# Performance work log

Hardware: AMD Instinct MI355X
Metric: run time of the kernel (lower is better)

The kernel has to match this reference:

```python
import jax, jax.numpy as jnp
import numpy as np

NUM_HEADS = 16
HEAD_DIM = 64
INPUT_DIM = 1024
EMBED_DIM = NUM_HEADS * HEAD_DIM  # 1024


def setup_inputs() -> dict:
    key = jax.random.key(0)
    ks = jax.random.split(key, 9)
    B, S = 4, 2048
    scale = 1.0 / np.sqrt(INPUT_DIM)
    return {
        "q": jax.random.normal(ks[0], (B, S, INPUT_DIM), dtype=jnp.float32),
        "k": jax.random.normal(ks[1], (B, S, INPUT_DIM), dtype=jnp.float32),
        "v": jax.random.normal(ks[2], (B, S, INPUT_DIM), dtype=jnp.float32),
        "Wq": jax.random.normal(ks[3], (INPUT_DIM, EMBED_DIM), dtype=jnp.float32) * scale,
        "bq": jax.random.normal(ks[4], (EMBED_DIM,), dtype=jnp.float32) * 0.02,
        "Wk": jax.random.normal(ks[5], (INPUT_DIM, EMBED_DIM), dtype=jnp.float32) * scale,
        "bk": jax.random.normal(ks[6], (EMBED_DIM,), dtype=jnp.float32) * 0.02,
        "Wv": jax.random.normal(ks[7], (INPUT_DIM, EMBED_DIM), dtype=jnp.float32) * scale,
        "bv": jax.random.normal(ks[8], (EMBED_DIM,), dtype=jnp.float32) * 0.02,
    }


def reference(q, k, v, Wq, bq, Wk, bk, Wv, bv):
    B, Sq, _ = q.shape
    Sk = k.shape[1]
    # QKV projections (dropout_prob=0 -> identity; ReLU on value path)
    query = (q @ Wq + bq).reshape(B, Sq, NUM_HEADS, HEAD_DIM).transpose(0, 2, 1, 3)  # [B,H,Sq,D]
    key_ = (k @ Wk + bk).reshape(B, Sk, NUM_HEADS, HEAD_DIM).transpose(0, 2, 1, 3)   # [B,H,Sk,D]
    value = jax.nn.relu(v @ Wv + bv).reshape(B, Sk, NUM_HEADS, HEAD_DIM).transpose(0, 2, 1, 3)
    scores = jnp.einsum("bhqd,bhkd->bhqk", query, key_) / np.sqrt(HEAD_DIM).astype(np.float32)
    p_attn = jax.nn.softmax(scores, axis=-1)
    x = jnp.einsum("bhqk,bhkd->bhqd", p_attn, value)  # [B,H,Sq,D]
    return x.transpose(0, 2, 1, 3).reshape(B, Sq, EMBED_DIM)
```

## Files before the change

### kernel.cpp

```cpp
#include <hip/hip_runtime.h>
#include <hip/hip_bf16.h>
#include <stdint.h>

#define BB    4
#define NH    16
#define SEQ   2048
#define DH    64
#define EMB   1024
#define KD    1024
#define MROWS 8192

typedef short  short8  __attribute__((ext_vector_type(8)));
typedef float  f32x4   __attribute__((ext_vector_type(4)));
typedef float  f32x16  __attribute__((ext_vector_type(16)));

typedef const __attribute__((address_space(1))) void* gas_t;
typedef __attribute__((address_space(3))) void*       las_t;
#define GLD16(g, l) __builtin_amdgcn_global_load_lds((gas_t)(g), (las_t)(l), 16, 0, 0)

__device__ __forceinline__ unsigned short f2bf(float f) {
    unsigned u = __float_as_uint(f);
    u += 0x7fffu + ((u >> 16) & 1u);
    return (unsigned short)(u >> 16);
}
__device__ __forceinline__ unsigned packbf(float lo, float hi) {
    union { __hip_bfloat162 h; unsigned u; } cv;
    cv.h = __float22bfloat162_rn(make_float2(lo, hi));
    return cv.u;
}

__global__ __launch_bounds__(256) void wt_kernel(const float* __restrict__ Wq,
                                                 const float* __restrict__ Wk,
                                                 const float* __restrict__ Wv,
                                                 unsigned short* __restrict__ Wt) {
    __shared__ float tsh[64 * 68];
    const int p = blockIdx.z;
    const float* W = (p == 0) ? Wq : (p == 1) ? Wk : Wv;
    unsigned short* dst = Wt + (size_t)p * (KD * EMB);
    const int k0 = blockIdx.x * 64, n0 = blockIdx.y * 64;
    const int t = threadIdx.x;
    {
        const int r = t >> 2, c4 = (t & 3) * 16;
        const float* g = W + (size_t)(k0 + r) * EMB + n0 + c4;
        float* row = &tsh[r * 68 + c4];
        *(float4*)(row + 0)  = *(const float4*)(g + 0);
        *(float4*)(row + 4)  = *(const float4*)(g + 4);
        *(float4*)(row + 8)  = *(const float4*)(g + 8);
        *(float4*)(row + 12) = *(const float4*)(g + 12);
    }
    __syncthreads();
    {
        const int j = t >> 2, kp = (t & 3) * 16;
        unsigned ub[8];
#pragma unroll
        for (int ii = 0; ii < 8; ++ii)
            ub[ii] = packbf(tsh[(kp + 2 * ii) * 68 + j], tsh[(kp + 2 * ii + 1) * 68 + j]);
        unsigned short* o = dst + (size_t)(n0 + j) * KD + k0 + kp;
        *(uint4*)(o + 0) = uint4{ub[0], ub[1], ub[2], ub[3]};
        *(uint4*)(o + 8) = uint4{ub[4], ub[5], ub[6], ub[7]};
    }
}

__global__ __launch_bounds__(256) void proj_kernel(
    const float* __restrict__ qf, const float* __restrict__ kf,
    const float* __restrict__ vf, const unsigned short* __restrict__ WtBase,
    const float* __restrict__ bq, const float* __restrict__ bk, const float* __restrict__ bv,
    unsigned short* __restrict__ Qg, unsigned short* __restrict__ Kg,
    unsigned short* __restrict__ Vt)
{
    __shared__ __align__(16) unsigned short smem[17408];
    unsigned short* Ash = smem;
    unsigned short* Bsh = smem + 8192;

    const int p = blockIdx.z;
    const float* Af = (p == 0) ? qf : (p == 1) ? kf : vf;
    const unsigned short* Wp  = WtBase  + (size_t)p * (KD * EMB);
    const float* bias = (p == 0) ? bq : (p == 1) ? bk : bv;
    unsigned short* dst = (p == 0) ? Qg : (p == 1) ? Kg : Vt;

    const int row0 = blockIdx.x * 128;
    const int col0 = blockIdx.y * 128;
    const int t = threadIdx.x, lane = t & 63, wv = t >> 6;
    const int ln15 = lane & 15, q4 = lane >> 4;
    const int wm = wv & 1, wn = wv >> 1;

    f32x4 acc[4][4];
#pragma unroll
    for (int i = 0; i < 4; ++i)
#pragma unroll
        for (int j = 0; j < 4; ++j)
#pragma unroll
            for (int r = 0; r < 4; ++r) acc[i][j][r] = 0.f;

    const int lr = lane >> 3, lc = (lane & 7) ^ lr;
    const float*          gAf = Af + (size_t)(row0 + wv * 32 + lr) * KD + lc * 8;
    const unsigned short* gB  = Wp + (size_t)(col0 + wv * 32 + lr) * KD + lc * 8;
    unsigned short* lA = Ash + wv * 32 * 64;
    unsigned short* lB = Bsh + wv * 32 * 64;

    for (int k0 = 0; k0 < KD; k0 += 64) {
#pragma unroll
        for (int i = 0; i < 4; ++i) {
            GLD16(gB + (size_t)i * 8 * KD + k0, lB + i * 512);
            float4 a0 = *(const float4*)(gAf + (size_t)i * 8 * KD + k0);
            float4 a1 = *(const float4*)(gAf + (size_t)i * 8 * KD + k0 + 4);
            uint4 u;
            u.x = packbf(a0.x, a0.y); u.y = packbf(a0.z, a0.w);
            u.z = packbf(a1.x, a1.y); u.w = packbf(a1.z, a1.w);
            *(uint4*)&lA[i * 512 + lane * 8] = u;
        }
        __syncthreads();
#pragma unroll
        for (int kk = 0; kk < 2; ++kk) {
            short8 af[4], bfr[4];
#pragma unroll
            for (int mi = 0; mi < 4; ++mi) {
                const int r = wm * 64 + mi * 16 + ln15;
                af[mi] = *(const short8*)&Ash[r * 64 + (((kk << 2) | q4) ^ (r & 7)) * 8];
            }
#pragma unroll
            for (int ni = 0; ni < 4; ++ni) {
                const int r = wn * 64 + ni * 16 + ln15;
                bfr[ni] = *(const short8*)&Bsh[r * 64 + (((kk << 2) | q4) ^ (r & 7)) * 8];
            }
#pragma unroll
            for (int mi = 0; mi < 4; ++mi)
#pragma unroll
                for (int ni = 0; ni < 4; ++ni)
                    acc[mi][ni] = __builtin_amdgcn_mfma_f32_16x16x32_bf16(
                        af[mi], bfr[ni], acc[mi][ni], 0, 0, 0);
        }
        __syncthreads();
    }

    float bvv[4];
#pragma unroll
    for (int ni = 0; ni < 4; ++ni) bvv[ni] = bias[col0 + wn * 64 + ni * 16 + ln15];
    const float scq = 0.18033688011112042f;

    unsigned short* Tsh = smem;
#pragma unroll
    for (int mi = 0; mi < 4; ++mi)
#pragma unroll
        for (int ni = 0; ni < 4; ++ni)
#pragma unroll
            for (int r = 0; r < 4; ++r) {
                const int mr = wm * 64 + mi * 16 + q4 * 4 + r;
                const int ec = wn * 64 + ni * 16 + ln15;
                float vv = acc[mi][ni][r] + bvv[ni];
                if (p == 0) vv *= scq;
                if (p == 2) vv = vv > 0.f ? vv : 0.f;
                Tsh[mr * 136 + ec] = f2bf(vv);
            }
    __syncthreads();

    if (p < 2) {
        const int mr = t >> 1, hsel = t & 1;
        const int m = row0 + mr, bi = m >> 11, s = m & 2047;
        const int hh = (col0 >> 6) + hsel;
        const unsigned short* src = &Tsh[mr * 136 + hsel * 64];
        unsigned short* o = dst + ((size_t)(bi * NH + hh) * SEQ + s) * DH;
#pragma unroll
        for (int c = 0; c < 8; ++c)
            *(uint4*)(o + 8 * c) = *(const uint4*)(src + 8 * c);
    } else {
        const int e = t >> 1, sh2 = t & 1;
        const int n = col0 + e, hh = n >> 6, dd = n & 63;
        const int bi = row0 >> 11, sbase = (row0 & 2047) + sh2 * 64;
        unsigned ub[32];
#pragma unroll
        for (int i = 0; i < 32; ++i)
            ub[i] = (unsigned)Tsh[(sh2 * 64 + 2 * i) * 136 + e] |
                    ((unsigned)Tsh[(sh2 * 64 + 2 * i + 1) * 136 + e] << 16);
        unsigned short* o = dst + ((size_t)(bi * NH + hh) * DH + dd) * SEQ + sbase;
#pragma unroll
        for (int c = 0; c < 8; ++c)
            *(uint4*)(o + 8 * c) = uint4{ub[4 * c], ub[4 * c + 1], ub[4 * c + 2], ub[4 * c + 3]};
    }
}

__global__ __launch_bounds__(512) void attn_kernel(
    const unsigned short* __restrict__ Qg, const unsigned short* __restrict__ Kg,
    const unsigned short* __restrict__ Vt, float* __restrict__ out)
{
    __shared__ __align__(16) unsigned short smem[18432];

    const int lin = blockIdx.x + (blockIdx.y << 3) + (blockIdx.z << 7);
    const int g_xcd = lin & 7, s_lin = lin >> 3;
    const int qb = s_lin & 7;
    const int bh_idx = g_xcd + ((s_lin >> 3) << 3);
    const int hh = bh_idx & 15, bb = bh_idx >> 4;

    const int t = threadIdx.x, lane = t & 63, wv = t >> 6;
    const int ln31 = lane & 31, h2 = lane >> 5;
    const size_t bh = (size_t)(bb * NH + hh);
    const unsigned short* Qp = Qg + bh * (SEQ * DH);
    const unsigned short* Kp = Kg + bh * (SEQ * DH);
    const unsigned short* Vp = Vt + bh * (DH * SEQ);
    const int q0 = qb * 256 + wv * 32;

    short8 qf[4];
#pragma unroll
    for (int dc = 0; dc < 4; ++dc)
        qf[dc] = *(const short8*)(Qp + (size_t)(q0 + ln31) * DH + h2 * 8 + dc * 16);

    short8 ones;
#pragma unroll
    for (int i = 0; i < 8; ++i) ones[i] = (short)0x3F80;

    f32x16 accO[2], accL;
#pragma unroll
    for (int i = 0; i < 16; ++i) { accO[0][i] = 0.f; accO[1][i] = 0.f; accL[i] = 0.f; }

    const int srow = t >> 3, sp = (t & 7) * 8;
    const int prow = srow ^ (((((srow >> 2) ^ (srow >> 3)) & 1)) ? 12 : 0);
    const unsigned short* gk = Kp + (size_t)srow * DH + sp;
    const unsigned short* gv = Vp + (size_t)srow * SEQ + sp;
    const int wkoff = prow * 72 + sp;
    const int wvoff = 4608 + srow * 72 + sp;

    {
        short8 ka = *(const short8*)(gk);
        short8 va = *(const short8*)(gv);
        *(short8*)&smem[wkoff] = ka;
        *(short8*)&smem[wvoff] = va;
    }

    for (int it = 0; it < 32; ++it) {
        const int nxt = (it + 1) & 31;
        short8 ka = *(const short8*)(gk + (size_t)nxt * 64 * DH);
        short8 va = *(const short8*)(gv + nxt * 64);

        __syncthreads();

        const unsigned short* Ksh = smem + (it & 1) * 9216;
        const unsigned short* Vsh = Ksh + 4608;

        f32x16 st[2];
#pragma unroll
        for (int kt = 0; kt < 2; ++kt) {
#pragma unroll
            for (int i = 0; i < 16; ++i) st[kt][i] = 0.f;
#pragma unroll
            for (int dc = 0; dc < 4; ++dc) {
                short8 kf = *(const short8*)&Ksh[(kt * 32 + ln31) * 72 + h2 * 8 + dc * 16];
                st[kt] = __builtin_amdgcn_mfma_f32_32x32x16_bf16(kf, qf[dc], st[kt], 0, 0, 0);
            }
        }
#pragma unroll
        for (int kt = 0; kt < 2; ++kt)
#pragma unroll
            for (int r = 0; r < 16; ++r)
                st[kt][r] = __builtin_amdgcn_exp2f(st[kt][r]);

#pragma unroll
        for (int kt = 0; kt < 2; ++kt)
#pragma unroll
            for (int kc = 0; kc < 2; ++kc) {
                union { unsigned u[4]; short8 v; } pf;
#pragma unroll
                for (int i = 0; i < 4; ++i)
                    pf.u[i] = packbf(st[kt][8 * kc + 2 * i], st[kt][8 * kc + 2 * i + 1]);
                accL = __builtin_amdgcn_mfma_f32_32x32x16_bf16(ones, pf.v, accL, 0, 0, 0);
#pragma unroll
                for (int dt = 0; dt < 2; ++dt) {
                    short8 vf = *(const short8*)&Vsh[(dt * 32 + ln31) * 72 + kt * 32 + kc * 16 + h2 * 8];
                    accO[dt] = __builtin_amdgcn_mfma_f32_32x32x16_bf16(vf, pf.v, accO[dt], 0, 0, 0);
                }
            }

        unsigned short* wbuf = smem + ((it + 1) & 1) * 9216;
        *(short8*)&wbuf[wkoff] = ka;
        *(short8*)&wbuf[wvoff] = va;
    }

    const float inv = 1.0f / accL[0];
    float* orow = out + ((size_t)(bb * SEQ + q0 + ln31) * NH + hh) * 64;
#pragma unroll
    for (int dt = 0; dt < 2; ++dt)
#pragma unroll
        for (int g = 0; g < 4; ++g) {
            float4 w;
            w.x = accO[dt][4 * g + 0] * inv;
            w.y = accO[dt][4 * g + 1] * inv;
            w.z = accO[dt][4 * g + 2] * inv;
            w.w = accO[dt][4 * g + 3] * inv;
            *(float4*)(orow + dt * 32 + 4 * h2 + 8 * g) = w;
        }
}

extern "C" void kernel_launch(void* const* d_in, const int* in_sizes, int n_in,
                              void* d_out, int out_size, void* d_ws, size_t ws_size,
                              hipStream_t stream) {
    const float* qf = (const float*)d_in[0];
    const float* kf = (const float*)d_in[1];
    const float* vf = (const float*)d_in[2];
    const float* Wq = (const float*)d_in[3];
    const float* bq = (const float*)d_in[4];
    const float* Wk = (const float*)d_in[5];
    const float* bk = (const float*)d_in[6];
    const float* Wv = (const float*)d_in[7];
    const float* bv = (const float*)d_in[8];

    char* ws = (char*)d_ws;
    unsigned short* Wt  = (unsigned short*)ws;
    unsigned short* Qg  = (unsigned short*)(ws + 6291456);
    unsigned short* Kg  = Qg + 8388608;
    unsigned short* Vt  = Kg + 8388608;
    float* out = (float*)d_out;

    wt_kernel<<<dim3(16, 16, 3), 256, 0, stream>>>(Wq, Wk, Wv, Wt);
    proj_kernel<<<dim3(64, 8, 3), 256, 0, stream>>>(qf, kf, vf, Wt, bq, bk, bv, Qg, Kg, Vt);
    attn_kernel<<<dim3(8, 16, 4), 512, 0, stream>>>(Qg, Kg, Vt, out);
}
```

Measured before the change: 306.1 us.

## Double-buffer LDS and prefetch fp32 A tiles two steps ahead in projection GEMM

Reworks the projection GEMM main loop to ping-pong between two LDS buffers. Weight tiles for the next k-step are loaded asynchronously, and fp32 activations are prefetched into registers two steps ahead and converted to bf16 one step ahead. This overlaps global loads with MFMA work and drops one barrier per iteration. In exchange it doubles shared memory to 64 KB per block and raises register pressure from the prefetch arrays, which may lower occupancy.

```diff
diff --git a/kernel.cpp b/kernel.cpp
--- a/kernel.cpp
+++ b/kernel.cpp
@@ -68,9 +68,7 @@
     unsigned short* __restrict__ Qg, unsigned short* __restrict__ Kg,
     unsigned short* __restrict__ Vt)
 {
-    __shared__ __align__(16) unsigned short smem[17408];
-    unsigned short* Ash = smem;
-    unsigned short* Bsh = smem + 8192;
+    __shared__ __align__(16) unsigned short smem[32768];
 
     const int p = blockIdx.z;
     const float* Af = (p == 0) ? qf : (p == 1) ? kf : vf;
@@ -95,33 +93,55 @@
     const int lr = lane >> 3, lc = (lane & 7) ^ lr;
     const float*          gAf = Af + (size_t)(row0 + wv * 32 + lr) * KD + lc * 8;
     const unsigned short* gB  = Wp + (size_t)(col0 + wv * 32 + lr) * KD + lc * 8;
-    unsigned short* lA = Ash + wv * 32 * 64;
-    unsigned short* lB = Bsh + wv * 32 * 64;
-
-    for (int k0 = 0; k0 < KD; k0 += 64) {
+    const int lAoff = wv * 2048 + lane * 8;
+    const int lBoff = 8192 + wv * 2048;
+
+    float4 aN[4][2];
+    float4 aF[4][2];
+
+    {
+        float4 a0[4][2];
 #pragma unroll
         for (int i = 0; i < 4; ++i) {
-            GLD16(gB + (size_t)i * 8 * KD + k0, lB + i * 512);
-            float4 a0 = *(const float4*)(gAf + (size_t)i * 8 * KD + k0);
-            float4 a1 = *(const float4*)(gAf + (size_t)i * 8 * KD + k0 + 4);
+            a0[i][0] = *(const float4*)(gAf + (size_t)i * 8 * KD + 0);
+            a0[i][1] = *(const float4*)(gAf + (size_t)i * 8 * KD + 4);
+        }
+#pragma unroll
+        for (int i = 0; i < 4; ++i)
+            GLD16(gB + (size_t)i * 8 * KD + 0, smem + lBoff + i * 512);
+#pragma unroll
+        for (int i = 0; i < 4; ++i) {
             uint4 u;
-            u.x = packbf(a0.x, a0.y); u.y = packbf(a0.z, a0.w);
-            u.z = packbf(a1.x, a1.y); u.w = packbf(a1.z, a1.w);
-            *(uint4*)&lA[i * 512 + lane * 8] = u;
-        }
+            u.x = packbf(a0[i][0].x, a0[i][0].y); u.y = packbf(a0[i][0].z, a0[i][0].w);
+            u.z = packbf(a0[i][1].x, a0[i][1].y); u.w = packbf(a0[i][1].z, a0[i][1].w);
+            *(uint4*)&smem[lAoff + i * 512] = u;
+        }
+#pragma unroll
+        for (int i = 0; i < 4; ++i) {
+            aN[i][0] = *(const float4*)(gAf + (size_t)i * 8 * KD + 64);
+            aN[i][1] = *(const float4*)(gAf + (size_t)i * 8 * KD + 64 + 4);
+        }
+    }
+
+#pragma unroll
+    for (int k0 = 0; k0 < 16; ++k0) {
         __syncthreads();
+
+        const unsigned short* Ab_ = smem + (k0 & 1) * 16384;
+        const unsigned short* Bb_ = Ab_ + 8192;
+
 #pragma unroll
         for (int kk = 0; kk < 2; ++kk) {
             short8 af[4], bfr[4];
 #pragma unroll
             for (int mi = 0; mi < 4; ++mi) {
                 const int r = wm * 64 + mi * 16 + ln15;
-                af[mi] = *(const short8*)&Ash[r * 64 + (((kk << 2) | q4) ^ (r & 7)) * 8];
+                af[mi] = *(const short8*)&Ab_[r * 64 + (((kk << 2) | q4) ^ (r & 7)) * 8];
             }
 #pragma unroll
             for (int ni = 0; ni < 4; ++ni) {
                 const int r = wn * 64 + ni * 16 + ln15;
-                bfr[ni] = *(const short8*)&Bsh[r * 64 + (((kk << 2) | q4) ^ (r & 7)) * 8];
+                bfr[ni] = *(const short8*)&Bb_[r * 64 + (((kk << 2) | q4) ^ (r & 7)) * 8];
             }
 #pragma unroll
             for (int mi = 0; mi < 4; ++mi)
@@ -130,8 +150,31 @@
                     acc[mi][ni] = __builtin_amdgcn_mfma_f32_16x16x32_bf16(
                         af[mi], bfr[ni], acc[mi][ni], 0, 0, 0);
         }
-        __syncthreads();
-    }
+
+        if (k0 < 15) {
+            unsigned short* dBuf = smem + ((k0 + 1) & 1) * 16384;
+#pragma unroll
+            for (int i = 0; i < 4; ++i)
+                GLD16(gB + (size_t)i * 8 * KD + (k0 + 1) * 64, dBuf + lBoff + i * 512);
+            if (k0 < 14) {
+#pragma unroll
+                for (int i = 0; i < 4; ++i) {
+                    aF[i][0] = *(const float4*)(gAf + (size_t)i * 8 * KD + (k0 + 2) * 64);
+                    aF[i][1] = *(const float4*)(gAf + (size_t)i * 8 * KD + (k0 + 2) * 64 + 4);
+                }
+            }
+#pragma unroll
+            for (int i = 0; i < 4; ++i) {
+                uint4 u;
+                u.x = packbf(aN[i][0].x, aN[i][0].y); u.y = packbf(aN[i][0].z, aN[i][0].w);
+                u.z = packbf(aN[i][1].x, aN[i][1].y); u.w = packbf(aN[i][1].z, aN[i][1].w);
+                *(uint4*)&dBuf[lAoff + i * 512] = u;
+            }
+#pragma unroll
+            for (int i = 0; i < 4; ++i) { aN[i][0] = aF[i][0]; aN[i][1] = aF[i][1]; }
+        }
+    }
+    __syncthreads();
 
     float bvv[4];
 #pragma unroll
```

New measurement: 321.7 us. +5.1%, slower.

## Widen projection GEMM tile to 128x256 with 512 threads

Applied to the files above, without the earlier changes.

The projection kernel now computes a 128x256 output tile per block with 8 waves instead of 128x128 with 4 waves. The fp32 activation tile, converted to bf16, is shared across twice as many output columns, which halves redundant reads and conversions of the A operand. The epilogue writes the tile back in two 128-column halves through shared memory. In exchange the grid has half as many blocks and uses more LDS per block, which may lower occupancy and add extra syncs in the epilogue.

```diff
diff --git a/kernel.cpp b/kernel.cpp
--- a/kernel.cpp
+++ b/kernel.cpp
@@ -61,14 +61,14 @@
     }
 }
 
-__global__ __launch_bounds__(256) void proj_kernel(
+__global__ __launch_bounds__(512) void proj_kernel(
     const float* __restrict__ qf, const float* __restrict__ kf,
     const float* __restrict__ vf, const unsigned short* __restrict__ WtBase,
     const float* __restrict__ bq, const float* __restrict__ bk, const float* __restrict__ bv,
     unsigned short* __restrict__ Qg, unsigned short* __restrict__ Kg,
     unsigned short* __restrict__ Vt)
 {
-    __shared__ __align__(16) unsigned short smem[17408];
+    __shared__ __align__(16) unsigned short smem[24576];
     unsigned short* Ash = smem;
     unsigned short* Bsh = smem + 8192;
 
@@ -79,10 +79,11 @@
     unsigned short* dst = (p == 0) ? Qg : (p == 1) ? Kg : Vt;
 
     const int row0 = blockIdx.x * 128;
-    const int col0 = blockIdx.y * 128;
+    const int col0 = blockIdx.y * 256;
     const int t = threadIdx.x, lane = t & 63, wv = t >> 6;
     const int ln15 = lane & 15, q4 = lane >> 4;
     const int wm = wv & 1, wn = wv >> 1;
+    const int wva = wv >> 1;
 
     f32x4 acc[4][4];
 #pragma unroll
@@ -93,23 +94,26 @@
             for (int r = 0; r < 4; ++r) acc[i][j][r] = 0.f;
 
     const int lr = lane >> 3, lc = (lane & 7) ^ lr;
-    const float*          gAf = Af + (size_t)(row0 + wv * 32 + lr) * KD + lc * 8;
+    const float*          gAf = Af + (size_t)(row0 + wva * 32 + lr) * KD + lc * 8;
     const unsigned short* gB  = Wp + (size_t)(col0 + wv * 32 + lr) * KD + lc * 8;
-    unsigned short* lA = Ash + wv * 32 * 64;
     unsigned short* lB = Bsh + wv * 32 * 64;
 
     for (int k0 = 0; k0 < KD; k0 += 64) {
 #pragma unroll
-        for (int i = 0; i < 4; ++i) {
+        for (int i = 0; i < 4; ++i)
             GLD16(gB + (size_t)i * 8 * KD + k0, lB + i * 512);
-            float4 a0 = *(const float4*)(gAf + (size_t)i * 8 * KD + k0);
-            float4 a1 = *(const float4*)(gAf + (size_t)i * 8 * KD + k0 + 4);
+#pragma unroll
+        for (int j = 0; j < 2; ++j) {
+            const int i2 = (wv & 1) * 2 + j;
+            float4 a0 = *(const float4*)(gAf + (size_t)i2 * 8 * KD + k0);
+            float4 a1 = *(const float4*)(gAf + (size_t)i2 * 8 * KD + k0 + 4);
             uint4 u;
             u.x = packbf(a0.x, a0.y); u.y = packbf(a0.z, a0.w);
             u.z = packbf(a1.x, a1.y); u.w = packbf(a1.z, a1.w);
-            *(uint4*)&lA[i * 512 + lane * 8] = u;
-        }
-        __syncthreads();
+            *(uint4*)&Ash[wva * 2048 + i2 * 512 + lane * 8] = u;
+        }
+        __syncthreads();
+
 #pragma unroll
         for (int kk = 0; kk < 2; ++kk) {
             short8 af[4], bfr[4];
@@ -140,42 +144,50 @@
 
     unsigned short* Tsh = smem;
 #pragma unroll
-    for (int mi = 0; mi < 4; ++mi)
-#pragma unroll
-        for (int ni = 0; ni < 4; ++ni)
-#pragma unroll
-            for (int r = 0; r < 4; ++r) {
-                const int mr = wm * 64 + mi * 16 + q4 * 4 + r;
-                const int ec = wn * 64 + ni * 16 + ln15;
-                float vv = acc[mi][ni][r] + bvv[ni];
-                if (p == 0) vv *= scq;
-                if (p == 2) vv = vv > 0.f ? vv : 0.f;
-                Tsh[mr * 136 + ec] = f2bf(vv);
-            }
-    __syncthreads();
-
-    if (p < 2) {
-        const int mr = t >> 1, hsel = t & 1;
-        const int m = row0 + mr, bi = m >> 11, s = m & 2047;
-        const int hh = (col0 >> 6) + hsel;
-        const unsigned short* src = &Tsh[mr * 136 + hsel * 64];
-        unsigned short* o = dst + ((size_t)(bi * NH + hh) * SEQ + s) * DH;
-#pragma unroll
-        for (int c = 0; c < 8; ++c)
-            *(uint4*)(o + 8 * c) = *(const uint4*)(src + 8 * c);
-    } else {
-        const int e = t >> 1, sh2 = t & 1;
-        const int n = col0 + e, hh = n >> 6, dd = n & 63;
-        const int bi = row0 >> 11, sbase = (row0 & 2047) + sh2 * 64;
-        unsigned ub[32];
-#pragma unroll
-        for (int i = 0; i < 32; ++i)
-            ub[i] = (unsigned)Tsh[(sh2 * 64 + 2 * i) * 136 + e] |
-                    ((unsigned)Tsh[(sh2 * 64 + 2 * i + 1) * 136 + e] << 16);
-        unsigned short* o = dst + ((size_t)(bi * NH + hh) * DH + dd) * SEQ + sbase;
-#pragma unroll
-        for (int c = 0; c < 8; ++c)
-            *(uint4*)(o + 8 * c) = uint4{ub[4 * c], ub[4 * c + 1], ub[4 * c + 2], ub[4 * c + 3]};
+    for (int h = 0; h < 2; ++h) {
+        __syncthreads();
+        if ((wn >> 1) == h) {
+            const int ecb = (wn & 1) * 64;
+#pragma unroll
+            for (int mi = 0; mi < 4; ++mi)
+#pragma unroll
+                for (int ni = 0; ni < 4; ++ni)
+#pragma unroll
+                    for (int r = 0; r < 4; ++r) {
+                        const int mr = wm * 64 + mi * 16 + q4 * 4 + r;
+                        const int ec = ecb + ni * 16 + ln15;
+                        float vv = acc[mi][ni][r] + bvv[ni];
+                        if (p == 0) vv *= scq;
+                        if (p == 2) vv = vv > 0.f ? vv : 0.f;
+                        Tsh[mr * 136 + ec] = f2bf(vv);
+                    }
+        }
+        __syncthreads();
+
+        if (p < 2) {
+            const int mr = t >> 2, sub = t & 3, hsel = sub >> 1, qtr = sub & 1;
+            const int m = row0 + mr, bi = m >> 11, s = m & 2047;
+            const int hh = (col0 >> 6) + h * 2 + hsel;
+            const unsigned short* src = &Tsh[mr * 136 + hsel * 64 + qtr * 32];
+            unsigned short* o = dst + ((size_t)(bi * NH + hh) * SEQ + s) * DH + qtr * 32;
+#pragma unroll
+            for (int c = 0; c < 4; ++c)
+                *(uint4*)(o + 8 * c) = *(const uint4*)(src + 8 * c);
+        } else {
+            const int e = t >> 2, sub = t & 3, sh2 = sub >> 1, qtr = sub & 1;
+            const int n = col0 + h * 128 + e, hhv = n >> 6, dd = n & 63;
+            const int bi = row0 >> 11;
+            const int sbase = (row0 & 2047) + sh2 * 64 + qtr * 32;
+            unsigned ub[16];
+#pragma unroll
+            for (int i = 0; i < 16; ++i)
+                ub[i] = (unsigned)Tsh[(sh2 * 64 + qtr * 32 + 2 * i) * 136 + e] |
+                        ((unsigned)Tsh[(sh2 * 64 + qtr * 32 + 2 * i + 1) * 136 + e] << 16);
+            unsigned short* o = dst + ((size_t)(bi * NH + hhv) * DH + dd) * SEQ + sbase;
+#pragma unroll
+            for (int c = 0; c < 4; ++c)
+                *(uint4*)(o + 8 * c) = uint4{ub[4 * c], ub[4 * c + 1], ub[4 * c + 2], ub[4 * c + 3]};
+        }
     }
 }
 
@@ -310,6 +322,6 @@
     float* out = (float*)d_out;
 
     wt_kernel<<<dim3(16, 16, 3), 256, 0, stream>>>(Wq, Wk, Wv, Wt);
-    proj_kernel<<<dim3(64, 8, 3), 256, 0, stream>>>(qf, kf, vf, Wt, bq, bk, bv, Qg, Kg, Vt);
+    proj_kernel<<<dim3(64, 4, 3), 512, 0, stream>>>(qf, kf, vf, Wt, bq, bk, bv, Qg, Kg, Vt);
     attn_kernel<<<dim3(8, 16, 4), 512, 0, stream>>>(Qg, Kg, Vt, out);
 }
```

Measured after the change: 303.8 us. No clear change (-0.8%).
